# Kernel tuning notes

Measured on AMD Instinct MI355X. Metric: run time of the kernel, lower is better.

Reference implementation:

```python
import jax, jax.numpy as jnp
import numpy as np
from jax import lax

D_MODEL = 1024
EXPAND = 2
D_INNER = EXPAND * D_MODEL        # 2048
D_STATE = 16
D_CONV = 4
DT_RANK = (D_MODEL + 15) // 16    # 64, standard 'auto' dt_rank
BATCH, SEQ = 2, 1024


def setup_inputs() -> dict:
    key = jax.random.key(0)
    ks = jax.random.split(key, 10)
    g = lambda k, shape, sc: jax.random.normal(k, shape, jnp.float32) * sc
    A_log = jnp.log(jnp.broadcast_to(
        jnp.arange(1, D_STATE + 1, dtype=jnp.float32), (D_INNER, D_STATE)))
    return {
        "x": jax.random.normal(ks[0], (BATCH, SEQ, D_MODEL), jnp.float32),
        "gamma": jnp.ones((D_MODEL,), jnp.float32),
        "beta": jnp.zeros((D_MODEL,), jnp.float32),
        "W_in": g(ks[1], (D_MODEL, 2 * D_INNER), 0.02),
        "W_conv": g(ks[2], (D_INNER, D_CONV), 0.1),
        "b_conv": jnp.zeros((D_INNER,), jnp.float32),
        "W_x": g(ks[3], (D_INNER, DT_RANK + 2 * D_STATE), 0.02),
        "W_dt": g(ks[4], (DT_RANK, D_INNER), 0.1),
        "b_dt": g(ks[5], (D_INNER,), 0.1),
        "A_log": A_log,
        "Dskip": jnp.ones((D_INNER,), jnp.float32),
        "W_out": g(ks[6], (D_INNER, D_MODEL), 0.02),
    }


def _layernorm(x, gamma, beta, eps=1e-5):
    mu = jnp.mean(x, axis=-1, keepdims=True)
    var = jnp.mean(jnp.square(x - mu), axis=-1, keepdims=True)
    return (x - mu) * lax.rsqrt(var + eps) * gamma + beta


def _mamba_block(x, gamma, beta, W_in, W_conv, b_conv, W_x, W_dt, b_dt,
                 A_log, Dskip, W_out):
    h = _layernorm(x, gamma, beta)                       # [B,L,D]
    xz = h @ W_in                                        # [B,L,2*Din]
    xi, z = jnp.split(xz, 2, axis=-1)                    # each [B,L,Din]

    # depthwise causal conv over time
    xt = xi.transpose(0, 2, 1)                           # [B,Din,L]
    conv = lax.conv_general_dilated(
        xt, W_conv[:, None, :], window_strides=(1,),
        padding=[(D_CONV - 1, 0)], feature_group_count=D_INNER)
    u = jax.nn.silu(conv + b_conv[None, :, None]).transpose(0, 2, 1)  # [B,L,Din]

    x_dbl = u @ W_x                                      # [B,L,dt_rank+2N]
    dt_r = x_dbl[..., :DT_RANK]
    Bm = x_dbl[..., DT_RANK:DT_RANK + D_STATE]           # [B,L,N]
    Cm = x_dbl[..., DT_RANK + D_STATE:]                  # [B,L,N]
    dt = jax.nn.softplus(dt_r @ W_dt + b_dt)             # [B,L,Din]

    A = -jnp.exp(A_log)                                  # [Din,N]

    def step(hstate, inp):
        dt_s, B_s, C_s, u_s = inp                        # [B,Din],[B,N],[B,N],[B,Din]
        dA = jnp.exp(dt_s[..., None] * A)                # [B,Din,N]
        hstate = dA * hstate + (dt_s * u_s)[..., None] * B_s[:, None, :]
        y = jnp.einsum('bdn,bn->bd', hstate, C_s)
        return hstate, y

    h0 = jnp.zeros((x.shape[0], D_INNER, D_STATE), x.dtype)
    _, ys = lax.scan(step, h0, (dt.transpose(1, 0, 2), Bm.transpose(1, 0, 2),
                                Cm.transpose(1, 0, 2), u.transpose(1, 0, 2)))
    y = ys.transpose(1, 0, 2) + u * Dskip                # [B,L,Din]
    y = y * jax.nn.silu(z)
    return x + y @ W_out                                 # residual


def reference(x, gamma, beta, W_in, W_conv, b_conv, W_x, W_dt, b_dt,
              A_log, Dskip, W_out):
    return _mamba_block(x, gamma, beta, W_in, W_conv, b_conv, W_x, W_dt,
                        b_dt, A_log, Dskip, W_out)
```

## Files before the change

kernel.cpp:

```cpp
#include <hip/hip_runtime.h>
#include <math.h>

#define BB 2
#define SS 1024
#define DM 1024
#define DI 2048
#define DSTATE 16
#define DTR 64
#define NX 96
#define ROWS (BB*SS)
#define NCHUNK 16
#define LC (SS/NCHUNK)
#define NCH (BB*DI)
#define TS 16
#define NT (LC/TS)
#define KSPLIT 4
#define KSX 16

typedef __bf16 bf16x8 __attribute__((ext_vector_type(8)));
typedef float f32x4 __attribute__((ext_vector_type(4)));

static __device__ __forceinline__ unsigned short f2bf(float f) {
    unsigned u = __builtin_bit_cast(unsigned, f);
    unsigned r = (u + 0x7fff + ((u >> 16) & 1)) >> 16;
    return (unsigned short)r;
}

__global__ __launch_bounds__(256) void ln_kernel(const float* __restrict__ x,
                                                 const float* __restrict__ gamma,
                                                 const float* __restrict__ beta,
                                                 unsigned short* __restrict__ h) {
    int row = blockIdx.x;
    const float* xr = x + (size_t)row * DM;
    float v[4];
    float s = 0.f;
#pragma unroll
    for (int i = 0; i < 4; i++) { v[i] = xr[threadIdx.x + i * 256]; s += v[i]; }
    __shared__ float red[4], red2[4];
    int lane = threadIdx.x & 63, wid = threadIdx.x >> 6;
#pragma unroll
    for (int m = 1; m < 64; m <<= 1) s += __shfl_xor(s, m);
    if (lane == 0) red[wid] = s;
    __syncthreads();
    float mean = (red[0] + red[1] + red[2] + red[3]) * (1.0f / DM);
    float vs = 0.f;
#pragma unroll
    for (int i = 0; i < 4; i++) { float dv = v[i] - mean; vs += dv * dv; }
#pragma unroll
    for (int m = 1; m < 64; m <<= 1) vs += __shfl_xor(vs, m);
    if (lane == 0) red2[wid] = vs;
    __syncthreads();
    float var = (red2[0] + red2[1] + red2[2] + red2[3]) * (1.0f / DM);
    float inv = rsqrtf(var + 1e-5f);
    unsigned short* hr = h + (size_t)row * DM;
#pragma unroll
    for (int i = 0; i < 4; i++) {
        int idx = threadIdx.x + i * 256;
        hr[idx] = f2bf((v[i] - mean) * inv * gamma[idx] + beta[idx]);
    }
}

__global__ __launch_bounds__(256) void transpose_bf16(const float* __restrict__ W,
                                                      unsigned short* __restrict__ WT,
                                                      int K, int N) {
    __shared__ unsigned short tile[32][33];
    int n0 = blockIdx.x * 32, k0 = blockIdx.y * 32;
    int tx = threadIdx.x & 31, ty = threadIdx.x >> 5;
#pragma unroll
    for (int r = 0; r < 4; r++)
        tile[ty + r * 8][tx] = f2bf(W[(size_t)(k0 + ty + r * 8) * N + n0 + tx]);
    __syncthreads();
#pragma unroll
    for (int r = 0; r < 4; r++)
        WT[(size_t)(n0 + ty + r * 8) * K + k0 + tx] = tile[tx][ty + r * 8];
}

__global__ __launch_bounds__(256) void gemm_mfma(const __bf16* __restrict__ A,
                                                 const __bf16* __restrict__ BT,
                                                 const float* __restrict__ resid,
                                                 float* __restrict__ C,
                                                 int M, int N, int K) {
    __shared__ __bf16 As[128 * 32];
    __shared__ __bf16 Bs[128 * 32];
    int tid = threadIdx.x;
    int w = tid >> 6, lane = tid & 63;
    int wr = w >> 1, wc = w & 1;
    int m0 = blockIdx.y * 128, n0 = blockIdx.x * 128;

    f32x4 acc[4][4] = {};

    int srow = lane >> 2;
    int sgran = lane & 3;
    const __bf16* gA = A + (size_t)(m0 + w * 32) * K;
    const __bf16* gB = BT + (size_t)(n0 + w * 32) * K;
    int fr = lane & 15, q = lane >> 4;

    for (int k0 = 0; k0 < K; k0 += 32) {
        __syncthreads();
#pragma unroll
        for (int c = 0; c < 2; c++) {
            const __bf16* ga = gA + (size_t)(c * 16 + srow) * K + k0 + sgran * 8;
            const __bf16* gb = gB + (size_t)(c * 16 + srow) * K + k0 + sgran * 8;
            __builtin_amdgcn_global_load_lds(
                (const __attribute__((address_space(1))) void*)ga,
                (__attribute__((address_space(3))) void*)&As[(w * 32 + c * 16) * 32], 16, 0, 0);
            __builtin_amdgcn_global_load_lds(
                (const __attribute__((address_space(1))) void*)gb,
                (__attribute__((address_space(3))) void*)&Bs[(w * 32 + c * 16) * 32], 16, 0, 0);
        }
        __syncthreads();
        bf16x8 af[4], bfr[4];
#pragma unroll
        for (int i = 0; i < 4; i++)
            af[i] = *(const bf16x8*)&As[(wr * 64 + i * 16 + fr) * 32 + q * 8];
#pragma unroll
        for (int j = 0; j < 4; j++)
            bfr[j] = *(const bf16x8*)&Bs[(wc * 64 + j * 16 + fr) * 32 + q * 8];
#pragma unroll
        for (int i = 0; i < 4; i++)
#pragma unroll
            for (int j = 0; j < 4; j++)
                acc[i][j] = __builtin_amdgcn_mfma_f32_16x16x32_bf16(af[i], bfr[j], acc[i][j], 0, 0, 0);
    }
#pragma unroll
    for (int i = 0; i < 4; i++) {
#pragma unroll
        for (int j = 0; j < 4; j++) {
#pragma unroll
            for (int r = 0; r < 4; r++) {
                size_t ro = (size_t)(m0 + wr * 64 + i * 16 + q * 4 + r) * N
                          + n0 + wc * 64 + j * 16 + fr;
                float v = acc[i][j][r];
                if (resid) v += resid[ro];
                C[ro] = v;
            }
        }
    }
}

__global__ __launch_bounds__(256) void gemm_mfma_splitk(const __bf16* __restrict__ A,
                                                        const __bf16* __restrict__ BT,
                                                        float* __restrict__ part,
                                                        int M, int N, int K) {
    __shared__ __bf16 As[128 * 32];
    __shared__ __bf16 Bs[128 * 32];
    int tid = threadIdx.x;
    int w = tid >> 6, lane = tid & 63;
    int wr = w >> 1, wc = w & 1;
    int m0 = blockIdx.y * 128, n0 = blockIdx.x * 128;
    int ks = K / KSPLIT;
    int kbase = blockIdx.z * ks;

    f32x4 acc[4][4] = {};
    int srow = lane >> 2, sgran = lane & 3;
    const __bf16* gA = A + (size_t)(m0 + w * 32) * K + kbase;
    const __bf16* gB = BT + (size_t)(n0 + w * 32) * K + kbase;
    int fr = lane & 15, q = lane >> 4;

    for (int k0 = 0; k0 < ks; k0 += 32) {
        __syncthreads();
#pragma unroll
        for (int c = 0; c < 2; c++) {
            const __bf16* ga = gA + (size_t)(c * 16 + srow) * K + k0 + sgran * 8;
            const __bf16* gb = gB + (size_t)(c * 16 + srow) * K + k0 + sgran * 8;
            __builtin_amdgcn_global_load_lds(
                (const __attribute__((address_space(1))) void*)ga,
                (__attribute__((address_space(3))) void*)&As[(w * 32 + c * 16) * 32], 16, 0, 0);
            __builtin_amdgcn_global_load_lds(
                (const __attribute__((address_space(1))) void*)gb,
                (__attribute__((address_space(3))) void*)&Bs[(w * 32 + c * 16) * 32], 16, 0, 0);
        }
        __syncthreads();
        bf16x8 af[4], bfr[4];
#pragma unroll
        for (int i = 0; i < 4; i++)
            af[i] = *(const bf16x8*)&As[(wr * 64 + i * 16 + fr) * 32 + q * 8];
#pragma unroll
        for (int j = 0; j < 4; j++)
            bfr[j] = *(const bf16x8*)&Bs[(wc * 64 + j * 16 + fr) * 32 + q * 8];
#pragma unroll
        for (int i = 0; i < 4; i++)
#pragma unroll
            for (int j = 0; j < 4; j++)
                acc[i][j] = __builtin_amdgcn_mfma_f32_16x16x32_bf16(af[i], bfr[j], acc[i][j], 0, 0, 0);
    }
    float* Cp = part + (size_t)blockIdx.z * M * N;
#pragma unroll
    for (int i = 0; i < 4; i++)
#pragma unroll
        for (int j = 0; j < 4; j++)
#pragma unroll
            for (int r = 0; r < 4; r++) {
                size_t ro = (size_t)(m0 + wr * 64 + i * 16 + q * 4 + r) * N
                          + n0 + wc * 64 + j * 16 + fr;
                Cp[ro] = acc[i][j][r];
            }
}

__global__ __launch_bounds__(256) void reduce_splitk(const float* __restrict__ part,
                                                     const float* __restrict__ x,
                                                     float* __restrict__ out) {
    size_t i4 = ((size_t)blockIdx.x * 256 + threadIdx.x) * 4;
    const size_t slice = (size_t)ROWS * DM;
    f32x4 s = *(const f32x4*)(x + i4);
#pragma unroll
    for (int z = 0; z < KSPLIT; z++) {
        f32x4 p = *(const f32x4*)(part + z * slice + i4);
        s.x += p.x; s.y += p.y; s.z += p.z; s.w += p.w;
    }
    *(f32x4*)(out + i4) = s;
}

__global__ __launch_bounds__(256) void gemm_mfma_xdbl(const __bf16* __restrict__ A,
                                                      const __bf16* __restrict__ BT,
                                                      float* __restrict__ part_x) {
    __shared__ __bf16 As[128 * 32];
    __shared__ __bf16 Bs[128 * 32];
    int tid = threadIdx.x;
    int w = tid >> 6, lane = tid & 63;
    int wr = w >> 1, wc = w & 1;
    int m0 = blockIdx.y * 128;
    int srow = lane >> 2, sgran = lane & 3;
    int fr = lane & 15, q = lane >> 4;
    f32x4 acc[4][4] = {};
    const int ks = DI / KSX;
    const int kbase = blockIdx.z * ks;
    const __bf16* gA = A + (size_t)(m0 + w * 32) * DI + kbase;

    for (int k0 = 0; k0 < ks; k0 += 32) {
        __syncthreads();
#pragma unroll
        for (int c = 0; c < 2; c++) {
            const __bf16* ga = gA + (size_t)(c * 16 + srow) * DI + k0 + sgran * 8;
            int brow = w * 32 + c * 16 + srow;
            if (brow > 95) brow = 95;
            const __bf16* gb = BT + (size_t)brow * DI + kbase + k0 + sgran * 8;
            __builtin_amdgcn_global_load_lds(
                (const __attribute__((address_space(1))) void*)ga,
                (__attribute__((address_space(3))) void*)&As[(w * 32 + c * 16) * 32], 16, 0, 0);
            __builtin_amdgcn_global_load_lds(
                (const __attribute__((address_space(1))) void*)gb,
                (__attribute__((address_space(3))) void*)&Bs[(w * 32 + c * 16) * 32], 16, 0, 0);
        }
        __syncthreads();
        bf16x8 af[4], bfr[4];
#pragma unroll
        for (int i = 0; i < 4; i++)
            af[i] = *(const bf16x8*)&As[(wr * 64 + i * 16 + fr) * 32 + q * 8];
#pragma unroll
        for (int j = 0; j < 4; j++)
            bfr[j] = *(const bf16x8*)&Bs[(wc * 64 + j * 16 + fr) * 32 + q * 8];
#pragma unroll
        for (int i = 0; i < 4; i++)
#pragma unroll
            for (int j = 0; j < 4; j++)
                acc[i][j] = __builtin_amdgcn_mfma_f32_16x16x32_bf16(af[i], bfr[j], acc[i][j], 0, 0, 0);
    }
    float* Cp = part_x + (size_t)blockIdx.z * ROWS * NX;
#pragma unroll
    for (int i = 0; i < 4; i++) {
#pragma unroll
        for (int j = 0; j < 4; j++) {
            int col = wc * 64 + j * 16 + fr;
            if (col < NX) {
#pragma unroll
                for (int r = 0; r < 4; r++) {
                    int row = m0 + wr * 64 + i * 16 + q * 4 + r;
                    Cp[(size_t)row * NX + col] = acc[i][j][r];
                }
            }
        }
    }
}

__global__ __launch_bounds__(256) void reduce_xdbl(const float* __restrict__ part_x,
                                                   float* __restrict__ xdbl,
                                                   unsigned short* __restrict__ dtr_bf) {
    int idx = blockIdx.x * 256 + threadIdx.x;
    const size_t slice = (size_t)ROWS * NX;
    float s = 0.f;
#pragma unroll
    for (int z = 0; z < KSX; z++) s += part_x[z * slice + idx];
    xdbl[idx] = s;
    int col = idx % NX;
    if (col < DTR) {
        int row = idx / NX;
        dtr_bf[(size_t)row * DTR + col] = f2bf(s);
    }
}

__global__ __launch_bounds__(256) void dt_gemm(const __bf16* __restrict__ A,
                                               const __bf16* __restrict__ BT,
                                               const float* __restrict__ b_dt,
                                               float* __restrict__ dt) {
    __shared__ __bf16 As[128 * 32];
    __shared__ __bf16 Bs[128 * 32];
    int tid = threadIdx.x;
    int w = tid >> 6, lane = tid & 63;
    int wr = w >> 1, wc = w & 1;
    int m0 = blockIdx.y * 128, n0 = blockIdx.x * 128;
    int srow = lane >> 2, sgran = lane & 3;
    int fr = lane & 15, q = lane >> 4;
    f32x4 acc[4][4] = {};
    const __bf16* gA = A + (size_t)(m0 + w * 32) * DTR;
    const __bf16* gB = BT + (size_t)(n0 + w * 32) * DTR;

    for (int k0 = 0; k0 < DTR; k0 += 32) {
        __syncthreads();
#pragma unroll
        for (int c = 0; c < 2; c++) {
            const __bf16* ga = gA + (size_t)(c * 16 + srow) * DTR + k0 + sgran * 8;
            const __bf16* gb = gB + (size_t)(c * 16 + srow) * DTR + k0 + sgran * 8;
            __builtin_amdgcn_global_load_lds(
                (const __attribute__((address_space(1))) void*)ga,
                (__attribute__((address_space(3))) void*)&As[(w * 32 + c * 16) * 32], 16, 0, 0);
            __builtin_amdgcn_global_load_lds(
                (const __attribute__((address_space(1))) void*)gb,
                (__attribute__((address_space(3))) void*)&Bs[(w * 32 + c * 16) * 32], 16, 0, 0);
        }
        __syncthreads();
        bf16x8 af[4], bfr[4];
#pragma unroll
        for (int i = 0; i < 4; i++)
            af[i] = *(const bf16x8*)&As[(wr * 64 + i * 16 + fr) * 32 + q * 8];
#pragma unroll
        for (int j = 0; j < 4; j++)
            bfr[j] = *(const bf16x8*)&Bs[(wc * 64 + j * 16 + fr) * 32 + q * 8];
#pragma unroll
        for (int i = 0; i < 4; i++)
#pragma unroll
            for (int j = 0; j < 4; j++)
                acc[i][j] = __builtin_amdgcn_mfma_f32_16x16x32_bf16(af[i], bfr[j], acc[i][j], 0, 0, 0);
    }
#pragma unroll
    for (int i = 0; i < 4; i++) {
#pragma unroll
        for (int j = 0; j < 4; j++) {
            int col = n0 + wc * 64 + j * 16 + fr;
            float bv = b_dt[col];
#pragma unroll
            for (int r = 0; r < 4; r++) {
                int row = m0 + wr * 64 + i * 16 + q * 4 + r;
                float a = acc[i][j][r] + bv;
                float sp = (a > 20.f) ? a : log1pf(expf(a));
                dt[(size_t)row * DI + col] = sp;
            }
        }
    }
}

__global__ __launch_bounds__(256) void conv_silu(const float* __restrict__ xz,
                                                 const float* __restrict__ Wc,
                                                 const float* __restrict__ bc,
                                                 float* __restrict__ u,
                                                 unsigned short* __restrict__ u_bf) {
    int idx = blockIdx.x * 256 + threadIdx.x;
    int d = idx & (DI - 1);
    int row = idx >> 11;
    int tpos = row & (SS - 1);
    float acc = bc[d];
#pragma unroll
    for (int k = 0; k < 4; k++) {
        int tt = tpos - 3 + k;
        if (tt >= 0) acc += xz[(size_t)(row - 3 + k) * (2 * DI) + d] * Wc[d * 4 + k];
    }
    float s = acc / (1.f + __expf(-acc));
    u[idx] = s;
    u_bf[idx] = f2bf(s);
}

__global__ __launch_bounds__(256) void scan_chunk1(const float* __restrict__ dt,
                                                   const float* __restrict__ u,
                                                   const float* __restrict__ xdbl,
                                                   const float* __restrict__ A_log,
                                                   float* __restrict__ Aprod,
                                                   float* __restrict__ hloc) {
    __shared__ float dts[TS * 256];
    __shared__ float us_[TS * 256];
    __shared__ float bs[LC * DSTATE];
    int tid = threadIdx.x;
    int d0 = blockIdx.x * 256;
    int db = d0 & (DI - 1);
    int j = blockIdx.y;
    int c = d0 + tid;
    int b = c >> 11;
    int d = c & (DI - 1);
    int w = tid >> 6, lane = tid & 63;
    size_t r0 = (size_t)b * SS + (size_t)j * LC;

    {
        int row = tid >> 2, col = (tid & 3) * 4;
        f32x4 v = *(const f32x4*)(xdbl + (r0 + row) * NX + DTR + col);
        *(f32x4*)&bs[row * DSTATE + col] = v;
    }
    float Av[DSTATE], h[DSTATE], P[DSTATE];
#pragma unroll
    for (int q = 0; q < 4; q++) {
        f32x4 al = *(const f32x4*)(A_log + (size_t)d * DSTATE + q * 4);
#pragma unroll
        for (int e = 0; e < 4; e++) {
            Av[q * 4 + e] = -expf(al[e]);
            h[q * 4 + e] = 0.f;
            P[q * 4 + e] = 1.f;
        }
    }

    for (int tile = 0; tile < NT; tile++) {
        int t0 = tile * TS;
#pragma unroll
        for (int i = 0; i < 4; i++) {
            int rl = w * 4 + i;
            const float* gdt = dt + (r0 + t0 + rl) * DI + db + lane * 4;
            const float* gu  = u  + (r0 + t0 + rl) * DI + db + lane * 4;
            __builtin_amdgcn_global_load_lds(
                (const __attribute__((address_space(1))) void*)gdt,
                (__attribute__((address_space(3))) void*)&dts[rl * 256], 16, 0, 0);
            __builtin_amdgcn_global_load_lds(
                (const __attribute__((address_space(1))) void*)gu,
                (__attribute__((address_space(3))) void*)&us_[rl * 256], 16, 0, 0);
        }
        __syncthreads();
#pragma unroll
        for (int t = 0; t < TS; t++) {
            float dtv = dts[t * 256 + tid];
            float uv  = us_[t * 256 + tid];
            float du = dtv * uv;
            const float* br = &bs[(t0 + t) * DSTATE];
            f32x4 Bq[4] = {*(const f32x4*)&br[0], *(const f32x4*)&br[4],
                           *(const f32x4*)&br[8], *(const f32x4*)&br[12]};
#pragma unroll
            for (int n = 0; n < DSTATE; n++) {
                float dA = __expf(dtv * Av[n]);
                P[n] *= dA;
                h[n] = dA * h[n] + du * Bq[n >> 2][n & 3];
            }
        }
        __syncthreads();
    }
    f32x4* Po = (f32x4*)(Aprod + ((size_t)j * NCH + c) * DSTATE);
    f32x4* ho = (f32x4*)(hloc + ((size_t)j * NCH + c) * DSTATE);
#pragma unroll
    for (int q = 0; q < 4; q++) {
        Po[q] = *(f32x4*)&P[q * 4];
        ho[q] = *(f32x4*)&h[q * 4];
    }
}

__global__ __launch_bounds__(256) void scan_combine(const float* __restrict__ Aprod,
                                                    const float* __restrict__ hloc,
                                                    float* __restrict__ h0arr) {
    int idx = blockIdx.x * 256 + threadIdx.x;
    float h = 0.f;
#pragma unroll
    for (int j = 0; j < NCHUNK; j++) {
        size_t o = (size_t)j * (NCH * DSTATE) + idx;
        h0arr[o] = h;
        h = Aprod[o] * h + hloc[o];
    }
}

__global__ __launch_bounds__(256) void scan_chunk2(const float* __restrict__ dt,
                                                   const float* __restrict__ u,
                                                   const float* __restrict__ xdbl,
                                                   const float* __restrict__ A_log,
                                                   const float* __restrict__ h0arr,
                                                   const float* __restrict__ xz,
                                                   const float* __restrict__ Dskip,
                                                   unsigned short* __restrict__ y2) {
    __shared__ float dts[TS * 256];
    __shared__ float us_[TS * 256];
    __shared__ float zs[TS * 256];
    __shared__ float bcs[LC * 2 * DSTATE];
    int tid = threadIdx.x;
    int d0 = blockIdx.x * 256;
    int db = d0 & (DI - 1);
    int j = blockIdx.y;
    int c = d0 + tid;
    int b = c >> 11;
    int d = c & (DI - 1);
    int w = tid >> 6, lane = tid & 63;
    size_t r0 = (size_t)b * SS + (size_t)j * LC;

    {
        int row = tid >> 2, col = (tid & 3) * 8;
        const float* src = xdbl + (r0 + row) * NX + DTR + col;
        f32x4 v0 = *(const f32x4*)src;
        f32x4 v1 = *(const f32x4*)(src + 4);
        *(f32x4*)&bcs[row * 32 + col] = v0;
        *(f32x4*)&bcs[row * 32 + col + 4] = v1;
    }
    float Av[DSTATE], h[DSTATE];
    const f32x4* h0p = (const f32x4*)(h0arr + ((size_t)j * NCH + c) * DSTATE);
#pragma unroll
    for (int q = 0; q < 4; q++) {
        f32x4 al = *(const f32x4*)(A_log + (size_t)d * DSTATE + q * 4);
        f32x4 h0v = h0p[q];
#pragma unroll
        for (int e = 0; e < 4; e++) {
            Av[q * 4 + e] = -expf(al[e]);
            h[q * 4 + e] = h0v[e];
        }
    }
    float Dv = Dskip[d];

    for (int tile = 0; tile < NT; tile++) {
        int t0 = tile * TS;
#pragma unroll
        for (int i = 0; i < 4; i++) {
            int rl = w * 4 + i;
            const float* gdt = dt + (r0 + t0 + rl) * DI + db + lane * 4;
            const float* gu  = u  + (r0 + t0 + rl) * DI + db + lane * 4;
            const float* gz  = xz + (r0 + t0 + rl) * (2 * DI) + DI + db + lane * 4;
            __builtin_amdgcn_global_load_lds(
                (const __attribute__((address_space(1))) void*)gdt,
                (__attribute__((address_space(3))) void*)&dts[rl * 256], 16, 0, 0);
            __builtin_amdgcn_global_load_lds(
                (const __attribute__((address_space(1))) void*)gu,
                (__attribute__((address_space(3))) void*)&us_[rl * 256], 16, 0, 0);
            __builtin_amdgcn_global_load_lds(
                (const __attribute__((address_space(1))) void*)gz,
                (__attribute__((address_space(3))) void*)&zs[rl * 256], 16, 0, 0);
        }
        __syncthreads();
#pragma unroll
        for (int t = 0; t < TS; t++) {
            float dtv = dts[t * 256 + tid];
            float uv  = us_[t * 256 + tid];
            float zz  = zs[t * 256 + tid];
            float du = dtv * uv;
            const float* br = &bcs[(t0 + t) * 32];
            f32x4 Bq[4] = {*(const f32x4*)&br[0], *(const f32x4*)&br[4],
                           *(const f32x4*)&br[8], *(const f32x4*)&br[12]};
            f32x4 Cq[4] = {*(const f32x4*)&br[16], *(const f32x4*)&br[20],
                           *(const f32x4*)&br[24], *(const f32x4*)&br[28]};
            float p = 0.f;
#pragma unroll
            for (int n = 0; n < DSTATE; n++) {
                float dA = __expf(dtv * Av[n]);
                h[n] = dA * h[n] + du * Bq[n >> 2][n & 3];
                p += h[n] * Cq[n >> 2][n & 3];
            }
            float sz = zz / (1.f + __expf(-zz));
            y2[(r0 + t0 + t) * DI + d] = f2bf((p + uv * Dv) * sz);
        }
        __syncthreads();
    }
}

extern "C" void kernel_launch(void* const* d_in, const int* in_sizes, int n_in,
                              void* d_out, int out_size, void* d_ws, size_t ws_size,
                              hipStream_t stream) {
    const float* x      = (const float*)d_in[0];
    const float* gamma  = (const float*)d_in[1];
    const float* beta   = (const float*)d_in[2];
    const float* W_in   = (const float*)d_in[3];
    const float* W_conv = (const float*)d_in[4];
    const float* b_conv = (const float*)d_in[5];
    const float* W_x    = (const float*)d_in[6];
    const float* W_dt   = (const float*)d_in[7];
    const float* b_dt   = (const float*)d_in[8];
    const float* A_log  = (const float*)d_in[9];
    const float* Dskip  = (const float*)d_in[10];
    const float* W_out  = (const float*)d_in[11];
    float* out = (float*)d_out;

    float* ws    = (float*)d_ws;
    float* xz    = ws;
    float* u     = xz + (size_t)ROWS * 2 * DI;
    float* xdbl  = u + (size_t)ROWS * DI;
    float* dt    = xdbl + (size_t)ROWS * NX;
    float* Aprod = dt + (size_t)ROWS * DI;
    float* hloc  = Aprod + (size_t)NCHUNK * NCH * DSTATE;
    float* h0arr = hloc + (size_t)NCHUNK * NCH * DSTATE;
    unsigned short* h_bf   = (unsigned short*)(h0arr + (size_t)NCHUNK * NCH * DSTATE);
    unsigned short* y_bf   = h_bf + (size_t)ROWS * DM;
    unsigned short* W_inT  = y_bf + (size_t)ROWS * DI;
    unsigned short* W_outT = W_inT + (size_t)(2 * DI) * DM;
    unsigned short* W_xT   = W_outT + (size_t)DM * DI;
    unsigned short* W_dtT  = W_xT + (size_t)NX * DI;
    unsigned short* dtr_bf = W_dtT + (size_t)DI * DTR;
    unsigned short* u_bf = W_inT;
    float* part = xz;
    float* part_x = dt;

    transpose_bf16<<<dim3(2 * DI / 32, DM / 32), 256, 0, stream>>>(W_in, W_inT, DM, 2 * DI);
    transpose_bf16<<<dim3(DM / 32, DI / 32), 256, 0, stream>>>(W_out, W_outT, DI, DM);
    transpose_bf16<<<dim3(NX / 32, DI / 32), 256, 0, stream>>>(W_x, W_xT, DI, NX);
    transpose_bf16<<<dim3(DI / 32, DTR / 32), 256, 0, stream>>>(W_dt, W_dtT, DTR, DI);
    ln_kernel<<<ROWS, 256, 0, stream>>>(x, gamma, beta, h_bf);
    gemm_mfma<<<dim3(2 * DI / 128, ROWS / 128), 256, 0, stream>>>(
        (const __bf16*)h_bf, (const __bf16*)W_inT, nullptr, xz, ROWS, 2 * DI, DM);
    conv_silu<<<ROWS * DI / 256, 256, 0, stream>>>(xz, W_conv, b_conv, u, u_bf);
    gemm_mfma_xdbl<<<dim3(1, ROWS / 128, KSX), 256, 0, stream>>>(
        (const __bf16*)u_bf, (const __bf16*)W_xT, part_x);
    reduce_xdbl<<<(ROWS * NX) / 256, 256, 0, stream>>>(part_x, xdbl, dtr_bf);
    dt_gemm<<<dim3(DI / 128, ROWS / 128), 256, 0, stream>>>(
        (const __bf16*)dtr_bf, (const __bf16*)W_dtT, b_dt, dt);
    scan_chunk1<<<dim3(NCH / 256, NCHUNK), 256, 0, stream>>>(dt, u, xdbl, A_log, Aprod, hloc);
    scan_combine<<<(NCH * DSTATE) / 256, 256, 0, stream>>>(Aprod, hloc, h0arr);
    scan_chunk2<<<dim3(NCH / 256, NCHUNK), 256, 0, stream>>>(dt, u, xdbl, A_log, h0arr,
                                                             xz, Dskip, y_bf);
    gemm_mfma_splitk<<<dim3(DM / 128, ROWS / 128, KSPLIT), 256, 0, stream>>>(
        (const __bf16*)y_bf, (const __bf16*)W_outT, part, ROWS, DM, DI);
    reduce_splitk<<<(ROWS * DM) / (256 * 4), 256, 0, stream>>>(part, x, out);
}
```

Measured before the change: 288.1 us.

## Store intermediates in bf16, merge prep kernels, fold scan combine into chunk2

```diff
diff --git a/kernel.cpp b/kernel.cpp
--- a/kernel.cpp
+++ b/kernel.cpp
@@ -26,45 +26,11 @@
     return (unsigned short)r;
 }
 
-__global__ __launch_bounds__(256) void ln_kernel(const float* __restrict__ x,
-                                                 const float* __restrict__ gamma,
-                                                 const float* __restrict__ beta,
-                                                 unsigned short* __restrict__ h) {
-    int row = blockIdx.x;
-    const float* xr = x + (size_t)row * DM;
-    float v[4];
-    float s = 0.f;
-#pragma unroll
-    for (int i = 0; i < 4; i++) { v[i] = xr[threadIdx.x + i * 256]; s += v[i]; }
-    __shared__ float red[4], red2[4];
-    int lane = threadIdx.x & 63, wid = threadIdx.x >> 6;
-#pragma unroll
-    for (int m = 1; m < 64; m <<= 1) s += __shfl_xor(s, m);
-    if (lane == 0) red[wid] = s;
-    __syncthreads();
-    float mean = (red[0] + red[1] + red[2] + red[3]) * (1.0f / DM);
-    float vs = 0.f;
-#pragma unroll
-    for (int i = 0; i < 4; i++) { float dv = v[i] - mean; vs += dv * dv; }
-#pragma unroll
-    for (int m = 1; m < 64; m <<= 1) vs += __shfl_xor(vs, m);
-    if (lane == 0) red2[wid] = vs;
-    __syncthreads();
-    float var = (red2[0] + red2[1] + red2[2] + red2[3]) * (1.0f / DM);
-    float inv = rsqrtf(var + 1e-5f);
-    unsigned short* hr = h + (size_t)row * DM;
-#pragma unroll
-    for (int i = 0; i < 4; i++) {
-        int idx = threadIdx.x + i * 256;
-        hr[idx] = f2bf((v[i] - mean) * inv * gamma[idx] + beta[idx]);
-    }
-}
-
-__global__ __launch_bounds__(256) void transpose_bf16(const float* __restrict__ W,
-                                                      unsigned short* __restrict__ WT,
-                                                      int K, int N) {
-    __shared__ unsigned short tile[32][33];
-    int n0 = blockIdx.x * 32, k0 = blockIdx.y * 32;
+__device__ __forceinline__ void transpose_body(const float* __restrict__ W,
+                                               unsigned short* __restrict__ WT,
+                                               int K, int N, int bx, int by,
+                                               unsigned short (*tile)[33]) {
+    int n0 = bx * 32, k0 = by * 32;
     int tx = threadIdx.x & 31, ty = threadIdx.x >> 5;
 #pragma unroll
     for (int r = 0; r < 4; r++)
@@ -75,22 +41,73 @@
         WT[(size_t)(n0 + ty + r * 8) * K + k0 + tx] = tile[tx][ty + r * 8];
 }
 
-__global__ __launch_bounds__(256) void gemm_mfma(const __bf16* __restrict__ A,
-                                                 const __bf16* __restrict__ BT,
-                                                 const float* __restrict__ resid,
-                                                 float* __restrict__ C,
-                                                 int M, int N, int K) {
+__global__ __launch_bounds__(256) void prep_kernel(const float* __restrict__ x,
+                                                   const float* __restrict__ gamma,
+                                                   const float* __restrict__ beta,
+                                                   unsigned short* __restrict__ h,
+                                                   const float* __restrict__ W_in,
+                                                   unsigned short* __restrict__ W_inT,
+                                                   const float* __restrict__ W_out,
+                                                   unsigned short* __restrict__ W_outT,
+                                                   const float* __restrict__ W_x,
+                                                   unsigned short* __restrict__ W_xT,
+                                                   const float* __restrict__ W_dt,
+                                                   unsigned short* __restrict__ W_dtT) {
+    __shared__ unsigned short tile[32][33];
+    __shared__ float red[4], red2[4];
+    int blk = blockIdx.x;
+    if (blk < ROWS) {
+        int row = blk;
+        const float* xr = x + (size_t)row * DM;
+        float v[4];
+        float s = 0.f;
+#pragma unroll
+        for (int i = 0; i < 4; i++) { v[i] = xr[threadIdx.x + i * 256]; s += v[i]; }
+        int lane = threadIdx.x & 63, wid = threadIdx.x >> 6;
+#pragma unroll
+        for (int m = 1; m < 64; m <<= 1) s += __shfl_xor(s, m);
+        if (lane == 0) red[wid] = s;
+        __syncthreads();
+        float mean = (red[0] + red[1] + red[2] + red[3]) * (1.0f / DM);
+        float vs = 0.f;
+#pragma unroll
+        for (int i = 0; i < 4; i++) { float dv = v[i] - mean; vs += dv * dv; }
+#pragma unroll
+        for (int m = 1; m < 64; m <<= 1) vs += __shfl_xor(vs, m);
+        if (lane == 0) red2[wid] = vs;
+        __syncthreads();
+        float var = (red2[0] + red2[1] + red2[2] + red2[3]) * (1.0f / DM);
+        float inv = rsqrtf(var + 1e-5f);
+        unsigned short* hr = h + (size_t)row * DM;
+#pragma unroll
+        for (int i = 0; i < 4; i++) {
+            int idx = threadIdx.x + i * 256;
+            hr[idx] = f2bf((v[i] - mean) * inv * gamma[idx] + beta[idx]);
+        }
+        return;
+    }
+    blk -= ROWS;
+    if (blk < 4096) { transpose_body(W_in, W_inT, DM, 2 * DI, blk % 128, blk / 128, tile); return; }
+    blk -= 4096;
+    if (blk < 2048) { transpose_body(W_out, W_outT, DI, DM, blk % 32, blk / 32, tile); return; }
+    blk -= 2048;
+    if (blk < 192) { transpose_body(W_x, W_xT, DI, NX, blk % 3, blk / 3, tile); return; }
+    blk -= 192;
+    transpose_body(W_dt, W_dtT, DTR, DI, blk % 64, blk / 64, tile);
+}
+
+__global__ __launch_bounds__(256) void gemm_mfma_bfout(const __bf16* __restrict__ A,
+                                                       const __bf16* __restrict__ BT,
+                                                       unsigned short* __restrict__ C,
+                                                       int M, int N, int K) {
     __shared__ __bf16 As[128 * 32];
     __shared__ __bf16 Bs[128 * 32];
     int tid = threadIdx.x;
     int w = tid >> 6, lane = tid & 63;
     int wr = w >> 1, wc = w & 1;
     int m0 = blockIdx.y * 128, n0 = blockIdx.x * 128;
-
     f32x4 acc[4][4] = {};
-
-    int srow = lane >> 2;
-    int sgran = lane & 3;
+    int srow = lane >> 2, sgran = lane & 3;
     const __bf16* gA = A + (size_t)(m0 + w * 32) * K;
     const __bf16* gB = BT + (size_t)(n0 + w * 32) * K;
     int fr = lane & 15, q = lane >> 4;
@@ -123,19 +140,15 @@
                 acc[i][j] = __builtin_amdgcn_mfma_f32_16x16x32_bf16(af[i], bfr[j], acc[i][j], 0, 0, 0);
     }
 #pragma unroll
-    for (int i = 0; i < 4; i++) {
-#pragma unroll
-        for (int j = 0; j < 4; j++) {
+    for (int i = 0; i < 4; i++)
+#pragma unroll
+        for (int j = 0; j < 4; j++)
 #pragma unroll
             for (int r = 0; r < 4; r++) {
                 size_t ro = (size_t)(m0 + wr * 64 + i * 16 + q * 4 + r) * N
                           + n0 + wc * 64 + j * 16 + fr;
-                float v = acc[i][j][r];
-                if (resid) v += resid[ro];
-                C[ro] = v;
+                C[ro] = f2bf(acc[i][j][r]);
             }
-        }
-    }
 }
 
 __global__ __launch_bounds__(256) void gemm_mfma_splitk(const __bf16* __restrict__ A,
@@ -150,7 +163,6 @@
     int m0 = blockIdx.y * 128, n0 = blockIdx.x * 128;
     int ks = K / KSPLIT;
     int kbase = blockIdx.z * ks;
-
     f32x4 acc[4][4] = {};
     int srow = lane >> 2, sgran = lane & 3;
     const __bf16* gA = A + (size_t)(m0 + w * 32) * K + kbase;
@@ -258,7 +270,7 @@
     }
     float* Cp = part_x + (size_t)blockIdx.z * ROWS * NX;
 #pragma unroll
-    for (int i = 0; i < 4; i++) {
+    for (int i = 0; i < 4; i++)
 #pragma unroll
         for (int j = 0; j < 4; j++) {
             int col = wc * 64 + j * 16 + fr;
@@ -270,7 +282,6 @@
                 }
             }
         }
-    }
 }
 
 __global__ __launch_bounds__(256) void reduce_xdbl(const float* __restrict__ part_x,
@@ -292,7 +303,7 @@
 __global__ __launch_bounds__(256) void dt_gemm(const __bf16* __restrict__ A,
                                                const __bf16* __restrict__ BT,
                                                const float* __restrict__ b_dt,
-                                               float* __restrict__ dt) {
+                                               unsigned short* __restrict__ dt) {
     __shared__ __bf16 As[128 * 32];
     __shared__ __bf16 Bs[128 * 32];
     int tid = threadIdx.x;
@@ -333,7 +344,7 @@
                 acc[i][j] = __builtin_amdgcn_mfma_f32_16x16x32_bf16(af[i], bfr[j], acc[i][j], 0, 0, 0);
     }
 #pragma unroll
-    for (int i = 0; i < 4; i++) {
+    for (int i = 0; i < 4; i++)
 #pragma unroll
         for (int j = 0; j < 4; j++) {
             int col = n0 + wc * 64 + j * 16 + fr;
@@ -343,16 +354,14 @@
                 int row = m0 + wr * 64 + i * 16 + q * 4 + r;
                 float a = acc[i][j][r] + bv;
                 float sp = (a > 20.f) ? a : log1pf(expf(a));
-                dt[(size_t)row * DI + col] = sp;
+                dt[(size_t)row * DI + col] = f2bf(sp);
             }
         }
-    }
-}
-
-__global__ __launch_bounds__(256) void conv_silu(const float* __restrict__ xz,
+}
+
+__global__ __launch_bounds__(256) void conv_silu(const __bf16* __restrict__ xz,
                                                  const float* __restrict__ Wc,
                                                  const float* __restrict__ bc,
-                                                 float* __restrict__ u,
                                                  unsigned short* __restrict__ u_bf) {
     int idx = blockIdx.x * 256 + threadIdx.x;
     int d = idx & (DI - 1);
@@ -362,21 +371,20 @@
 #pragma unroll
     for (int k = 0; k < 4; k++) {
         int tt = tpos - 3 + k;
-        if (tt >= 0) acc += xz[(size_t)(row - 3 + k) * (2 * DI) + d] * Wc[d * 4 + k];
+        if (tt >= 0) acc += (float)xz[(size_t)(row - 3 + k) * (2 * DI) + d] * Wc[d * 4 + k];
     }
     float s = acc / (1.f + __expf(-acc));
-    u[idx] = s;
     u_bf[idx] = f2bf(s);
 }
 
-__global__ __launch_bounds__(256) void scan_chunk1(const float* __restrict__ dt,
-                                                   const float* __restrict__ u,
+__global__ __launch_bounds__(256) void scan_chunk1(const __bf16* __restrict__ dt,
+                                                   const __bf16* __restrict__ u,
                                                    const float* __restrict__ xdbl,
                                                    const float* __restrict__ A_log,
                                                    float* __restrict__ Aprod,
                                                    float* __restrict__ hloc) {
-    __shared__ float dts[TS * 256];
-    __shared__ float us_[TS * 256];
+    __shared__ __bf16 dts[TS * 256];
+    __shared__ __bf16 us_[TS * 256];
     __shared__ float bs[LC * DSTATE];
     int tid = threadIdx.x;
     int d0 = blockIdx.x * 256;
@@ -386,6 +394,8 @@
     int b = c >> 11;
     int d = c & (DI - 1);
     int w = tid >> 6, lane = tid & 63;
+    int halfrow = lane >> 5;
+    int cw = (lane & 31) * 8;
     size_t r0 = (size_t)b * SS + (size_t)j * LC;
 
     {
@@ -408,10 +418,10 @@
     for (int tile = 0; tile < NT; tile++) {
         int t0 = tile * TS;
 #pragma unroll
-        for (int i = 0; i < 4; i++) {
-            int rl = w * 4 + i;
-            const float* gdt = dt + (r0 + t0 + rl) * DI + db + lane * 4;
-            const float* gu  = u  + (r0 + t0 + rl) * DI + db + lane * 4;
+        for (int i = 0; i < 2; i++) {
+            int rl = w * 4 + i * 2;
+            const __bf16* gdt = dt + (size_t)(r0 + t0 + rl + halfrow) * DI + db + cw;
+            const __bf16* gu  = u  + (size_t)(r0 + t0 + rl + halfrow) * DI + db + cw;
             __builtin_amdgcn_global_load_lds(
                 (const __attribute__((address_space(1))) void*)gdt,
                 (__attribute__((address_space(3))) void*)&dts[rl * 256], 16, 0, 0);
@@ -422,8 +432,8 @@
         __syncthreads();
 #pragma unroll
         for (int t = 0; t < TS; t++) {
-            float dtv = dts[t * 256 + tid];
-            float uv  = us_[t * 256 + tid];
+            float dtv = (float)dts[t * 256 + tid];
+            float uv  = (float)us_[t * 256 + tid];
             float du = dtv * uv;
             const float* br = &bs[(t0 + t) * DSTATE];
             f32x4 Bq[4] = {*(const f32x4*)&br[0], *(const f32x4*)&br[4],
@@ -446,30 +456,18 @@
     }
 }
 
-__global__ __launch_bounds__(256) void scan_combine(const float* __restrict__ Aprod,
-                                                    const float* __restrict__ hloc,
-                                                    float* __restrict__ h0arr) {
-    int idx = blockIdx.x * 256 + threadIdx.x;
-    float h = 0.f;
-#pragma unroll
-    for (int j = 0; j < NCHUNK; j++) {
-        size_t o = (size_t)j * (NCH * DSTATE) + idx;
-        h0arr[o] = h;
-        h = Aprod[o] * h + hloc[o];
-    }
-}
-
-__global__ __launch_bounds__(256) void scan_chunk2(const float* __restrict__ dt,
-                                                   const float* __restrict__ u,
+__global__ __launch_bounds__(256) void scan_chunk2(const __bf16* __restrict__ dt,
+                                                   const __bf16* __restrict__ u,
                                                    const float* __restrict__ xdbl,
                                                    const float* __restrict__ A_log,
-                                                   const float* __restrict__ h0arr,
-                                                   const float* __restrict__ xz,
+                                                   const float* __restrict__ Aprod,
+                                                   const float* __restrict__ hloc,
+                                                   const __bf16* __restrict__ xz,
                                                    const float* __restrict__ Dskip,
                                                    unsigned short* __restrict__ y2) {
-    __shared__ float dts[TS * 256];
-    __shared__ float us_[TS * 256];
-    __shared__ float zs[TS * 256];
+    __shared__ __bf16 dts[TS * 256];
+    __shared__ __bf16 us_[TS * 256];
+    __shared__ __bf16 zs[TS * 256];
     __shared__ float bcs[LC * 2 * DSTATE];
     int tid = threadIdx.x;
     int d0 = blockIdx.x * 256;
@@ -479,6 +477,8 @@
     int b = c >> 11;
     int d = c & (DI - 1);
     int w = tid >> 6, lane = tid & 63;
+    int halfrow = lane >> 5;
+    int cw = (lane & 31) * 8;
     size_t r0 = (size_t)b * SS + (size_t)j * LC;
 
     {
@@ -490,15 +490,24 @@
         *(f32x4*)&bcs[row * 32 + col + 4] = v1;
     }
     float Av[DSTATE], h[DSTATE];
-    const f32x4* h0p = (const f32x4*)(h0arr + ((size_t)j * NCH + c) * DSTATE);
 #pragma unroll
     for (int q = 0; q < 4; q++) {
         f32x4 al = *(const f32x4*)(A_log + (size_t)d * DSTATE + q * 4);
-        f32x4 h0v = h0p[q];
 #pragma unroll
         for (int e = 0; e < 4; e++) {
             Av[q * 4 + e] = -expf(al[e]);
-            h[q * 4 + e] = h0v[e];
+            h[q * 4 + e] = 0.f;
+        }
+    }
+    for (int jj = 0; jj < j; jj++) {
+        const f32x4* Pp = (const f32x4*)(Aprod + ((size_t)jj * NCH + c) * DSTATE);
+        const f32x4* Hp = (const f32x4*)(hloc + ((size_t)jj * NCH + c) * DSTATE);
+#pragma unroll
+        for (int q = 0; q < 4; q++) {
+            f32x4 P = Pp[q], H = Hp[q];
+#pragma unroll
+            for (int e = 0; e < 4; e++)
+                h[q * 4 + e] = P[e] * h[q * 4 + e] + H[e];
         }
     }
     float Dv = Dskip[d];
@@ -506,11 +515,11 @@
     for (int tile = 0; tile < NT; tile++) {
         int t0 = tile * TS;
 #pragma unroll
-        for (int i = 0; i < 4; i++) {
-            int rl = w * 4 + i;
-            const float* gdt = dt + (r0 + t0 + rl) * DI + db + lane * 4;
-            const float* gu  = u  + (r0 + t0 + rl) * DI + db + lane * 4;
-            const float* gz  = xz + (r0 + t0 + rl) * (2 * DI) + DI + db + lane * 4;
+        for (int i = 0; i < 2; i++) {
+            int rl = w * 4 + i * 2;
+            const __bf16* gdt = dt + (size_t)(r0 + t0 + rl + halfrow) * DI + db + cw;
+            const __bf16* gu  = u  + (size_t)(r0 + t0 + rl + halfrow) * DI + db + cw;
+            const __bf16* gz  = xz + (size_t)(r0 + t0 + rl + halfrow) * (2 * DI) + DI + db + cw;
             __builtin_amdgcn_global_load_lds(
                 (const __attribute__((address_space(1))) void*)gdt,
                 (__attribute__((address_space(3))) void*)&dts[rl * 256], 16, 0, 0);
@@ -524,9 +533,9 @@
         __syncthreads();
 #pragma unroll
         for (int t = 0; t < TS; t++) {
-            float dtv = dts[t * 256 + tid];
-            float uv  = us_[t * 256 + tid];
-            float zz  = zs[t * 256 + tid];
+            float dtv = (float)dts[t * 256 + tid];
+            float uv  = (float)us_[t * 256 + tid];
+            float zz  = (float)zs[t * 256 + tid];
             float du = dtv * uv;
             const float* br = &bcs[(t0 + t) * 32];
             f32x4 Bq[4] = {*(const f32x4*)&br[0], *(const f32x4*)&br[4],
@@ -564,42 +573,38 @@
     const float* W_out  = (const float*)d_in[11];
     float* out = (float*)d_out;
 
-    float* ws    = (float*)d_ws;
-    float* xz    = ws;
-    float* u     = xz + (size_t)ROWS * 2 * DI;
-    float* xdbl  = u + (size_t)ROWS * DI;
-    float* dt    = xdbl + (size_t)ROWS * NX;
-    float* Aprod = dt + (size_t)ROWS * DI;
-    float* hloc  = Aprod + (size_t)NCHUNK * NCH * DSTATE;
-    float* h0arr = hloc + (size_t)NCHUNK * NCH * DSTATE;
-    unsigned short* h_bf   = (unsigned short*)(h0arr + (size_t)NCHUNK * NCH * DSTATE);
+    float* ws     = (float*)d_ws;
+    float* xdbl   = ws;
+    float* Aprod  = xdbl + (size_t)ROWS * NX;
+    float* hloc   = Aprod + (size_t)NCHUNK * NCH * DSTATE;
+    float* part   = hloc + (size_t)NCHUNK * NCH * DSTATE;
+    float* part_x = part + (size_t)KSPLIT * ROWS * DM;
+    unsigned short* xz_bf  = (unsigned short*)(part_x + (size_t)KSX * ROWS * NX);
+    unsigned short* u_bf   = xz_bf + (size_t)ROWS * 2 * DI;
+    unsigned short* dt_bf  = u_bf + (size_t)ROWS * DI;
+    unsigned short* h_bf   = dt_bf + (size_t)ROWS * DI;
     unsigned short* y_bf   = h_bf + (size_t)ROWS * DM;
     unsigned short* W_inT  = y_bf + (size_t)ROWS * DI;
     unsigned short* W_outT = W_inT + (size_t)(2 * DI) * DM;
     unsigned short* W_xT   = W_outT + (size_t)DM * DI;
     unsigned short* W_dtT  = W_xT + (size_t)NX * DI;
     unsigned short* dtr_bf = W_dtT + (size_t)DI * DTR;
-    unsigned short* u_bf = W_inT;
-    float* part = xz;
-    float* part_x = dt;
-
-    transpose_bf16<<<dim3(2 * DI / 32, DM / 32), 256, 0, stream>>>(W_in, W_inT, DM, 2 * DI);
-    transpose_bf16<<<dim3(DM / 32, DI / 32), 256, 0, stream>>>(W_out, W_outT, DI, DM);
-    transpose_bf16<<<dim3(NX / 32, DI / 32), 256, 0, stream>>>(W_x, W_xT, DI, NX);
-    transpose_bf16<<<dim3(DI / 32, DTR / 32), 256, 0, stream>>>(W_dt, W_dtT, DTR, DI);
-    ln_kernel<<<ROWS, 256, 0, stream>>>(x, gamma, beta, h_bf);
-    gemm_mfma<<<dim3(2 * DI / 128, ROWS / 128), 256, 0, stream>>>(
-        (const __bf16*)h_bf, (const __bf16*)W_inT, nullptr, xz, ROWS, 2 * DI, DM);
-    conv_silu<<<ROWS * DI / 256, 256, 0, stream>>>(xz, W_conv, b_conv, u, u_bf);
+
+    prep_kernel<<<ROWS + 4096 + 2048 + 192 + 128, 256, 0, stream>>>(
+        x, gamma, beta, h_bf, W_in, W_inT, W_out, W_outT, W_x, W_xT, W_dt, W_dtT);
+    gemm_mfma_bfout<<<dim3(2 * DI / 128, ROWS / 128), 256, 0, stream>>>(
+        (const __bf16*)h_bf, (const __bf16*)W_inT, xz_bf, ROWS, 2 * DI, DM);
+    conv_silu<<<ROWS * DI / 256, 256, 0, stream>>>((const __bf16*)xz_bf, W_conv, b_conv, u_bf);
     gemm_mfma_xdbl<<<dim3(1, ROWS / 128, KSX), 256, 0, stream>>>(
         (const __bf16*)u_bf, (const __bf16*)W_xT, part_x);
     reduce_xdbl<<<(ROWS * NX) / 256, 256, 0, stream>>>(part_x, xdbl, dtr_bf);
     dt_gemm<<<dim3(DI / 128, ROWS / 128), 256, 0, stream>>>(
-        (const __bf16*)dtr_bf, (const __bf16*)W_dtT, b_dt, dt);
-    scan_chunk1<<<dim3(NCH / 256, NCHUNK), 256, 0, stream>>>(dt, u, xdbl, A_log, Aprod, hloc);
-    scan_combine<<<(NCH * DSTATE) / 256, 256, 0, stream>>>(Aprod, hloc, h0arr);
-    scan_chunk2<<<dim3(NCH / 256, NCHUNK), 256, 0, stream>>>(dt, u, xdbl, A_log, h0arr,
-                                                             xz, Dskip, y_bf);
+        (const __bf16*)dtr_bf, (const __bf16*)W_dtT, b_dt, dt_bf);
+    scan_chunk1<<<dim3(NCH / 256, NCHUNK), 256, 0, stream>>>(
+        (const __bf16*)dt_bf, (const __bf16*)u_bf, xdbl, A_log, Aprod, hloc);
+    scan_chunk2<<<dim3(NCH / 256, NCHUNK), 256, 0, stream>>>(
+        (const __bf16*)dt_bf, (const __bf16*)u_bf, xdbl, A_log, Aprod, hloc,
+        (const __bf16*)xz_bf, Dskip, y_bf);
     gemm_mfma_splitk<<<dim3(DM / 128, ROWS / 128, KSPLIT), 256, 0, stream>>>(
         (const __bf16*)y_bf, (const __bf16*)W_outT, part, ROWS, DM, DI);
     reduce_splitk<<<(ROWS * DM) / (256 * 4), 256, 0, stream>>>(part, x, out);
```

Measured after the change: 275.3 us. -4.4%, faster.
